# Performance work log

Hardware: AMD Instinct MI355X
Metric: run time of the kernel (lower is better)

Reference implementation:

```python
import jax, jax.numpy as jnp
import numpy as np
import math

WP, WF = 10, 10      # past/future window
EPS = 1e-8           # torch cosine_similarity eps
CLIP = 1.0 - 1e-6    # keep arccos (and its grad) finite
MAXN = 110           # hard-coded alpha width in the module


def setup_inputs() -> dict:
    key = jax.random.key(0)
    k1, k2, k3, k4, k5, k6 = jax.random.split(key, 6)
    B, L, G, N, D = 32, 110, 512, 40, 300
    node_features = jax.random.normal(k1, (B, L, G), jnp.float32)
    knowledge = jax.random.normal(k2, (B, L, N, D), jnp.float32)
    anew = jax.random.uniform(k3, (B, L, N), jnp.float32)
    var_sem = 2.0 / (G + G)
    var_con = 2.0 / (D + D)
    weight_sem = jax.random.normal(k4, (G, G), jnp.float32) * var_sem
    weight_con = jax.random.normal(k5, (D, D), jnp.float32) * var_con
    text_len = jax.random.randint(k6, (B,), 55, L + 1, jnp.int32)
    return dict(node_features=node_features, knowledge=knowledge, anew=anew,
                weight_sem=weight_sem, weight_con=weight_con, text_len=text_len)


def reference(node_features, knowledge, anew, weight_sem, weight_con, text_len):
    B, L, G = node_features.shape
    N = knowledge.shape[2]
    dt = node_features.dtype

    # window + validity mask, replaces per-(i,j) python slicing: [B, j, k]
    j = jnp.arange(L)[:, None]
    k = jnp.arange(L)[None, :]
    cur = text_len[:, None, None]
    mask = (k >= j - WP) & (k <= j + WF)
    mask = mask[None] & (k[None, :, :] <= cur - 1) & (j[None, :, :] < cur)
    fmask = mask.astype(dt)

    # ---- semantic branch: score = 1 - acos(cos_sim(f_j, W_sem f_k))/pi, windowed softmax
    att_sem = jnp.einsum('st,blt->bls', weight_sem, node_features)      # [B,L,G]
    num = jnp.einsum('bjg,bkg->bjk', node_features, att_sem)
    nf = jnp.maximum(jnp.linalg.norm(node_features, axis=-1), EPS)      # [B,L]
    na = jnp.maximum(jnp.linalg.norm(att_sem, axis=-1), EPS)            # [B,L]
    cos = num / (nf[:, :, None] * na[:, None, :])
    score = 1.0 - jnp.arccos(jnp.clip(cos, -CLIP, CLIP)) / math.pi
    neg = jnp.finfo(dt).min
    s = jnp.where(mask, score, neg)
    s = s - jnp.max(s, axis=-1, keepdims=True)
    e = jnp.exp(s) * fmask
    alphas_sem = e / jnp.maximum(jnp.sum(e, axis=-1, keepdims=True), EPS)  # [B,L,L]

    # ---- affinity transform of anew: v -> (||[v, v/2] - [0.5, 0]|| - 0.06467)/0.607468
    anew_aff = (jnp.sqrt((anew - 0.5) ** 2 + (0.5 * anew) ** 2) - 0.06467) / 0.607468

    # ---- contextual branch: windowed sum_n |cos_sim(aff_feat_{k,n}, knowledge_{j,n})|
    att_con = jnp.einsum('blns,st->blnt', knowledge, weight_con)        # [B,L,N,D]
    aff_feat = att_con * anew_aff[..., None]                            # [B,L,N,D]
    num_c = jnp.einsum('bknd,bjnd->bjkn', aff_feat, knowledge)          # [B,j,k,N]
    n_f = jnp.maximum(jnp.linalg.norm(aff_feat, axis=-1), EPS)          # [B,k,N]
    n_k = jnp.maximum(jnp.linalg.norm(knowledge, axis=-1), EPS)         # [B,j,N]
    cos_c = num_c / (n_f[:, None, :, :] * n_k[:, :, None, :])
    alphas_con = 10.0 * jnp.sum(jnp.abs(cos_c), axis=-1) * fmask        # [B,j,k]

    out = 0.5 * alphas_sem + 0.5 * alphas_con                           # [B,L,L]
    if L < MAXN:  # module hard-codes width 110
        out = jnp.pad(out, ((0, 0), (0, 0), (0, MAXN - L)))
    return out
```

## Files before the change

### kernel.cpp

```cpp
#include <hip/hip_runtime.h>
#include <hip/hip_bf16.h>
#include <math.h>

constexpr int Bb   = 32;
constexpr int Ls   = 110;
constexpr int Gs   = 512;
constexpr int Ns   = 40;
constexpr int Ds   = 300;
constexpr int WPc  = 10;
constexpr int WFc  = 10;
constexpr int MAXNc = 110;
constexpr float EPSf  = 1e-8f;
constexpr float CLIPf = 1.0f - 1e-6f;
constexpr int BL = Bb * Ls;
constexpr int Mrows = BL * Ns;

typedef __attribute__((ext_vector_type(8))) short short8_t;
typedef __attribute__((ext_vector_type(4))) short short4_t;
typedef __attribute__((ext_vector_type(4))) float floatx4;

__device__ __forceinline__ unsigned short bf16r(float f) {
  unsigned u = __float_as_uint(f);
  u += 0x7fffu + ((u >> 16) & 1u);
  return (unsigned short)(u >> 16);
}

__global__ __launch_bounds__(256) void transpose_wsem(const float* __restrict__ w,
                                                      float* __restrict__ wt) {
  __shared__ float tile[32][33];
  const int bx = blockIdx.x * 32;
  const int by = blockIdx.y * 32;
  const int tx = threadIdx.x;
  const int ty = threadIdx.y;
#pragma unroll
  for (int r = ty; r < 32; r += 8)
    tile[r][tx] = w[(by + r) * Gs + (bx + tx)];
  __syncthreads();
#pragma unroll
  for (int r = ty; r < 32; r += 8)
    wt[(bx + r) * Gs + (by + tx)] = tile[tx][r];
}

__global__ __launch_bounds__(256) void wct_prep(const float* __restrict__ wc,
                                                short* __restrict__ wct) {
  __shared__ float tile[32][33];
  const int t0 = blockIdx.x * 32;
  const int s0 = blockIdx.y * 32;
  const int tx = threadIdx.x, ty = threadIdx.y;
#pragma unroll
  for (int r = ty; r < 32; r += 8) {
    const int s = s0 + r, t = t0 + tx;
    tile[r][tx] = (s < Ds && t < Ds) ? wc[s * Ds + t] : 0.f;
  }
  __syncthreads();
#pragma unroll
  for (int r = ty; r < 32; r += 8) {
    const int t = t0 + r, s = s0 + tx;
    wct[t * 320 + s] = (short)bf16r(tile[tx][r]);
  }
}

__global__ __launch_bounds__(512) void sem_gemm(const float* __restrict__ nf,
                                                const float* __restrict__ wt,
                                                float* __restrict__ att_sem,
                                                float* __restrict__ na_arr) {
  const int bl0 = blockIdx.x * 8;
  const int s = threadIdx.x;
  const float* __restrict__ x0 = nf + (size_t)bl0 * Gs;
  float acc[8];
#pragma unroll
  for (int r = 0; r < 8; ++r) acc[r] = 0.f;
#pragma unroll 4
  for (int t = 0; t < Gs; ++t) {
    const float wv = wt[t * Gs + s];
#pragma unroll
    for (int r = 0; r < 8; ++r) acc[r] = fmaf(wv, x0[r * Gs + t], acc[r]);
  }
#pragma unroll
  for (int r = 0; r < 8; ++r) att_sem[(size_t)(bl0 + r) * Gs + s] = acc[r];

  __shared__ float partial[8][8];
  const int wave = s >> 6, lane = s & 63;
#pragma unroll
  for (int r = 0; r < 8; ++r) {
    float v = acc[r] * acc[r];
#pragma unroll
    for (int off = 32; off > 0; off >>= 1) v += __shfl_xor(v, off);
    if (lane == 0) partial[r][wave] = v;
  }
  __syncthreads();
  if (s < 8) {
    float sum = 0.f;
#pragma unroll
    for (int w2 = 0; w2 < 8; ++w2) sum += partial[s][w2];
    na_arr[bl0 + s] = fmaxf(sqrtf(sum), EPSf);
  }
}

__global__ __launch_bounds__(256) void sem_attn(const float* __restrict__ nf,
                                                const float* __restrict__ att_sem,
                                                const float* __restrict__ na_arr,
                                                const int* __restrict__ tlen,
                                                float* __restrict__ out) {
  const int blk = blockIdx.x;
  const int b = blk / Ls, j = blk % Ls;
  const int len = tlen[b];
  float* __restrict__ orow = out + (size_t)(b * Ls + j) * MAXNc;
  if (j >= len) {
    for (int k = threadIdx.x; k < MAXNc; k += 256) orow[k] = 0.f;
    return;
  }
  const int k0 = max(j - WPc, 0);
  const int k1 = min(j + WFc, len - 1);
  const int nk = k1 - k0 + 1;

  __shared__ float xs[Gs];
  __shared__ float sc[21];
  __shared__ float red[4];

  const float* __restrict__ x = nf + (size_t)(b * Ls + j) * Gs;
  float ss = 0.f;
  for (int t = threadIdx.x; t < Gs; t += 256) {
    const float v = x[t];
    xs[t] = v;
    ss += v * v;
  }
  const int wave = threadIdx.x >> 6, lane = threadIdx.x & 63;
#pragma unroll
  for (int off = 32; off > 0; off >>= 1) ss += __shfl_xor(ss, off);
  if (lane == 0) red[wave] = ss;
  __syncthreads();
  const float nfn = fmaxf(sqrtf(red[0] + red[1] + red[2] + red[3]), EPSf);

  for (int i = wave; i < nk; i += 4) {
    const int k = k0 + i;
    const float* __restrict__ as = att_sem + (size_t)(b * Ls + k) * Gs;
    float d = 0.f;
#pragma unroll
    for (int t = lane; t < Gs; t += 64) d = fmaf(xs[t], as[t], d);
#pragma unroll
    for (int off = 32; off > 0; off >>= 1) d += __shfl_xor(d, off);
    if (lane == 0) {
      float cs = d / (nfn * na_arr[b * Ls + k]);
      cs = fminf(fmaxf(cs, -CLIPf), CLIPf);
      sc[i] = 1.0f - acosf(cs) * (float)(1.0 / M_PI);
    }
  }
  __syncthreads();
  if (threadIdx.x == 0) {
    float m = -1e30f;
    for (int i = 0; i < nk; ++i) m = fmaxf(m, sc[i]);
    red[0] = m;
  }
  __syncthreads();
  const float m = red[0];
  if ((int)threadIdx.x < nk) sc[threadIdx.x] = expf(sc[threadIdx.x] - m);
  __syncthreads();
  if (threadIdx.x == 0) {
    float s = 0.f;
    for (int i = 0; i < nk; ++i) s += sc[i];
    red[1] = 1.0f / fmaxf(s, EPSf);
  }
  __syncthreads();
  const float inv = red[1];
  for (int k = threadIdx.x; k < MAXNc; k += 256) {
    float v = 0.f;
    if (k >= k0 && k <= k1) v = 0.5f * sc[k - k0] * inv;
    orow[k] = v;
  }
}

__global__ __launch_bounds__(256) void con_gemm_mfma(const float* __restrict__ kn,
                                                     const short* __restrict__ wct,
                                                     const float* __restrict__ anew,
                                                     const int* __restrict__ tlen,
                                                     unsigned short* __restrict__ ybar) {
  const int row0 = blockIdx.x * 64;
  {
    const int bl0 = row0 / Ns, bl1 = (row0 + 63) / Ns;
    bool alive = false;
    for (int bl = bl0; bl <= bl1; ++bl)
      if ((bl % Ls) < tlen[bl / Ls]) alive = true;
    if (!alive) return;
  }

  __shared__ short A_lds[64 * 40];
  __shared__ float rowss[64][4];
  __shared__ float scl[64];

  const int tid = threadIdx.x;
  const int wave = tid >> 6, lane = tid & 63;
  const int quad = lane >> 4, l16 = lane & 15;

  floatx4 acc[4][5];
#pragma unroll
  for (int mt = 0; mt < 4; ++mt)
#pragma unroll
    for (int i = 0; i < 5; ++i) acc[mt][i] = (floatx4){0.f, 0.f, 0.f, 0.f};

  const int r_st = tid >> 3;
  const int pos = tid & 7;

  for (int c = 0; c < 10; ++c) {
    const int k0 = c * 32 + pos * 4;
#pragma unroll
    for (int half = 0; half < 2; ++half) {
      const int r = r_st + half * 32;
      float4 v = make_float4(0.f, 0.f, 0.f, 0.f);
      if (k0 < Ds)
        v = *reinterpret_cast<const float4*>(kn + (size_t)(row0 + r) * Ds + k0);
      short4_t p;
      p.x = (short)bf16r(v.x);
      p.y = (short)bf16r(v.y);
      p.z = (short)bf16r(v.z);
      p.w = (short)bf16r(v.w);
      *reinterpret_cast<short4_t*>(&A_lds[r * 40 + pos * 4]) = p;
    }
    __syncthreads();

    short8_t bfrag[5];
#pragma unroll
    for (int i = 0; i < 5; ++i) {
      const int t = wave * 80 + i * 16 + l16;
      bfrag[i] = *reinterpret_cast<const short8_t*>(wct + t * 320 + c * 32 + quad * 8);
    }
#pragma unroll
    for (int mt = 0; mt < 4; ++mt) {
      const short8_t afrag =
          *reinterpret_cast<const short8_t*>(&A_lds[(mt * 16 + l16) * 40 + quad * 8]);
#pragma unroll
      for (int i = 0; i < 5; ++i)
        acc[mt][i] = __builtin_amdgcn_mfma_f32_16x16x32_bf16(afrag, bfrag[i], acc[mt][i], 0, 0, 0);
    }
    __syncthreads();
  }

#pragma unroll
  for (int mt = 0; mt < 4; ++mt) {
#pragma unroll
    for (int r = 0; r < 4; ++r) {
      float p = 0.f;
#pragma unroll
      for (int i = 0; i < 5; ++i) {
        const float y = acc[mt][i][r];
        p = fmaf(y, y, p);
      }
      p += __shfl_xor(p, 1);
      p += __shfl_xor(p, 2);
      p += __shfl_xor(p, 4);
      p += __shfl_xor(p, 8);
      if (l16 == 0) rowss[mt * 16 + quad * 4 + r][wave] = p;
    }
  }
  __syncthreads();
  if (tid < 64) {
    const float ss = rowss[tid][0] + rowss[tid][1] + rowss[tid][2] + rowss[tid][3];
    const float a = anew[row0 + tid];
    const float aff = (sqrtf((a - 0.5f) * (a - 0.5f) + 0.25f * a * a) - 0.06467f) *
                      (1.0f / 0.607468f);
    scl[tid] = aff / fmaxf(aff * sqrtf(ss), EPSf);
  }
  __syncthreads();

#pragma unroll
  for (int mt = 0; mt < 4; ++mt) {
#pragma unroll
    for (int i = 0; i < 5; ++i) {
      const int col = wave * 80 + i * 16 + l16;
      if (col < Ds) {
#pragma unroll
        for (int r = 0; r < 4; ++r) {
          const int row = mt * 16 + quad * 4 + r;
          ybar[(size_t)(row0 + row) * Ds + col] = bf16r(acc[mt][i][r] * scl[row]);
        }
      }
    }
  }
}

__global__ __launch_bounds__(512) void con_attn_mfma(const float* __restrict__ kn,
                                                     const unsigned short* __restrict__ ybar,
                                                     const int* __restrict__ tlen,
                                                     float* __restrict__ out) {
  const int b = blockIdx.x / 7;
  const int jt = blockIdx.x % 7;
  const int j0 = jt * 16;
  const int len = tlen[b];
  if (j0 >= len) return;
  const int kbase = min(max(j0 - WPc, 0), Ls - 48);

  const int tid = threadIdx.x;
  const int wave = tid >> 6, lane = tid & 63;
  const int quad = lane >> 4, l16 = lane & 15;

  __shared__ float red[8][768];

  const int jj = min(j0 + l16, Ls - 1);
  const size_t blj = (size_t)(b * Ls + jj);

  float outacc[3][4];
#pragma unroll
  for (int t = 0; t < 3; ++t)
#pragma unroll
    for (int r = 0; r < 4; ++r) outacc[t][r] = 0.f;

  const unsigned short* yrow[3];
#pragma unroll
  for (int t = 0; t < 3; ++t) {
    const int k = kbase + t * 16 + l16;
    yrow[t] = ybar + ((size_t)(b * Ls + k) * Ns) * Ds;
  }

  for (int ni = 0; ni < 5; ++ni) {
    const int n = wave + ni * 8;
    const float* __restrict__ arow = kn + (blj * Ns + n) * Ds;

    floatx4 S[3];
#pragma unroll
    for (int t = 0; t < 3; ++t) S[t] = (floatx4){0.f, 0.f, 0.f, 0.f};
    float ssq = 0.f;

#pragma unroll
    for (int c = 0; c < 10; ++c) {
      const int d0 = c * 32 + quad * 8;
      float av[8];
      if (c < 9) {
        const float4 v0 = *reinterpret_cast<const float4*>(arow + d0);
        const float4 v1 = *reinterpret_cast<const float4*>(arow + d0 + 4);
        av[0] = v0.x; av[1] = v0.y; av[2] = v0.z; av[3] = v0.w;
        av[4] = v1.x; av[5] = v1.y; av[6] = v1.z; av[7] = v1.w;
      } else {
        if (quad == 0) {
          const float4 v0 = *reinterpret_cast<const float4*>(arow + d0);
          const float4 v1 = *reinterpret_cast<const float4*>(arow + d0 + 4);
          av[0] = v0.x; av[1] = v0.y; av[2] = v0.z; av[3] = v0.w;
          av[4] = v1.x; av[5] = v1.y; av[6] = v1.z; av[7] = v1.w;
        } else if (quad == 1) {
          const float4 v0 = *reinterpret_cast<const float4*>(arow + d0);
          av[0] = v0.x; av[1] = v0.y; av[2] = v0.z; av[3] = v0.w;
          av[4] = av[5] = av[6] = av[7] = 0.f;
        } else {
#pragma unroll
          for (int e = 0; e < 8; ++e) av[e] = 0.f;
        }
      }
      short8_t afrag;
#pragma unroll
      for (int e = 0; e < 8; ++e) {
        ssq = fmaf(av[e], av[e], ssq);
        afrag[e] = (short)bf16r(av[e]);
      }
#pragma unroll
      for (int t = 0; t < 3; ++t) {
        const unsigned short* yr = yrow[t] + (size_t)n * Ds;
        short8_t bfrag;
        if (c < 9) {
          const short4_t u0 = *reinterpret_cast<const short4_t*>(yr + d0);
          const short4_t u1 = *reinterpret_cast<const short4_t*>(yr + d0 + 4);
          bfrag[0] = u0.x; bfrag[1] = u0.y; bfrag[2] = u0.z; bfrag[3] = u0.w;
          bfrag[4] = u1.x; bfrag[5] = u1.y; bfrag[6] = u1.z; bfrag[7] = u1.w;
        } else {
          if (quad == 0) {
            const short4_t u0 = *reinterpret_cast<const short4_t*>(yr + d0);
            const short4_t u1 = *reinterpret_cast<const short4_t*>(yr + d0 + 4);
            bfrag[0] = u0.x; bfrag[1] = u0.y; bfrag[2] = u0.z; bfrag[3] = u0.w;
            bfrag[4] = u1.x; bfrag[5] = u1.y; bfrag[6] = u1.z; bfrag[7] = u1.w;
          } else if (quad == 1) {
            const short4_t u0 = *reinterpret_cast<const short4_t*>(yr + d0);
            bfrag[0] = u0.x; bfrag[1] = u0.y; bfrag[2] = u0.z; bfrag[3] = u0.w;
            bfrag[4] = bfrag[5] = bfrag[6] = bfrag[7] = 0;
          } else {
#pragma unroll
            for (int e = 0; e < 8; ++e) bfrag[e] = 0;
          }
        }
        S[t] = __builtin_amdgcn_mfma_f32_16x16x32_bf16(afrag, bfrag, S[t], 0, 0, 0);
      }
    }

    ssq += __shfl_xor(ssq, 16);
    ssq += __shfl_xor(ssq, 32);
    const float kinv = 1.0f / fmaxf(sqrtf(ssq), EPSf);

#pragma unroll
    for (int r = 0; r < 4; ++r) {
      const float kv = __shfl(kinv, quad * 4 + r);
#pragma unroll
      for (int t = 0; t < 3; ++t)
        outacc[t][r] = fmaf(kv, fabsf(S[t][r]), outacc[t][r]);
    }
  }

#pragma unroll
  for (int t = 0; t < 3; ++t)
#pragma unroll
    for (int r = 0; r < 4; ++r)
      red[wave][(quad * 4 + r) * 48 + t * 16 + l16] = outacc[t][r];
  __syncthreads();

  for (int idx = tid; idx < 768; idx += 512) {
    float s = 0.f;
#pragma unroll
    for (int w = 0; w < 8; ++w) s += red[w][idx];
    const int j = j0 + idx / 48;
    const int k = kbase + idx % 48;
    if (j < len && k < len && k >= j - WPc && k <= j + WFc)
      out[(size_t)(b * Ls + j) * MAXNc + k] += 5.0f * s;
  }
}

extern "C" void kernel_launch(void* const* d_in, const int* in_sizes, int n_in,
                              void* d_out, int out_size, void* d_ws, size_t ws_size,
                              hipStream_t stream) {
  const float* nf   = (const float*)d_in[0];
  const float* kn   = (const float*)d_in[1];
  const float* anew = (const float*)d_in[2];
  const float* wsem = (const float*)d_in[3];
  const float* wcon = (const float*)d_in[4];
  const int*   tlen = (const int*)d_in[5];
  float* out = (float*)d_out;

  float* att_sem = (float*)d_ws;
  float* na_arr  = att_sem + (size_t)BL * Gs;
  float* wt      = na_arr + BL;
  short* wct     = (short*)(wt + (size_t)Gs * Gs);
  unsigned short* ybar = (unsigned short*)(wct + 320 * 320);

  transpose_wsem<<<dim3(16, 16), dim3(32, 8), 0, stream>>>(wsem, wt);
  wct_prep<<<dim3(10, 10), dim3(32, 8), 0, stream>>>(wcon, wct);
  sem_gemm<<<BL / 8, 512, 0, stream>>>(nf, wt, att_sem, na_arr);
  sem_attn<<<BL, 256, 0, stream>>>(nf, att_sem, na_arr, tlen, out);
  con_gemm_mfma<<<Mrows / 64, 256, 0, stream>>>(kn, wct, anew, tlen, ybar);
  con_attn_mfma<<<Bb * 7, 512, 0, stream>>>(kn, ybar, tlen, out);
}
```

Before: 508.2 us.

## Load con GEMM A fragments directly from global, drop LDS staging and barriers

The contextual GEMM kernel no longer stages the knowledge rows in shared memory. Each wave now loads its A fragments straight from global memory as float4 pairs and converts them to packed bf16 in registers. The K loop is split into nine full chunks plus a masked tail chunk, which removes both __syncthreads per iteration. In exchange, all four waves now redundantly read the same A rows from global/L2, and the per-lane loads are less coalesced.

```diff
diff --git a/kernel.cpp b/kernel.cpp
--- a/kernel.cpp
+++ b/kernel.cpp
@@ -25,6 +25,22 @@
   return (unsigned short)(u >> 16);
 }
 
+__device__ __forceinline__ unsigned pkbf(float lo, float hi) {
+  unsigned a = __float_as_uint(lo), b = __float_as_uint(hi);
+  a += 0x7fffu + ((a >> 16) & 1u);
+  b += 0x7fffu + ((b >> 16) & 1u);
+  return (a >> 16) | (b & 0xffff0000u);
+}
+
+__device__ __forceinline__ short8_t cvt8(const float4 v0, const float4 v1) {
+  union { short8_t s; unsigned u[4]; } p;
+  p.u[0] = pkbf(v0.x, v0.y);
+  p.u[1] = pkbf(v0.z, v0.w);
+  p.u[2] = pkbf(v1.x, v1.y);
+  p.u[3] = pkbf(v1.z, v1.w);
+  return p.s;
+}
+
 __global__ __launch_bounds__(256) void transpose_wsem(const float* __restrict__ w,
                                                       float* __restrict__ wt) {
   __shared__ float tile[32][33];
@@ -184,7 +200,6 @@
     if (!alive) return;
   }
 
-  __shared__ short A_lds[64 * 40];
   __shared__ float rowss[64][4];
   __shared__ float scl[64];
 
@@ -198,41 +213,54 @@
 #pragma unroll
     for (int i = 0; i < 5; ++i) acc[mt][i] = (floatx4){0.f, 0.f, 0.f, 0.f};
 
-  const int r_st = tid >> 3;
-  const int pos = tid & 7;
-
-  for (int c = 0; c < 10; ++c) {
-    const int k0 = c * 32 + pos * 4;
-#pragma unroll
-    for (int half = 0; half < 2; ++half) {
-      const int r = r_st + half * 32;
-      float4 v = make_float4(0.f, 0.f, 0.f, 0.f);
-      if (k0 < Ds)
-        v = *reinterpret_cast<const float4*>(kn + (size_t)(row0 + r) * Ds + k0);
-      short4_t p;
-      p.x = (short)bf16r(v.x);
-      p.y = (short)bf16r(v.y);
-      p.z = (short)bf16r(v.z);
-      p.w = (short)bf16r(v.w);
-      *reinterpret_cast<short4_t*>(&A_lds[r * 40 + pos * 4]) = p;
-    }
-    __syncthreads();
-
+  const float* arow[4];
+#pragma unroll
+  for (int mt = 0; mt < 4; ++mt)
+    arow[mt] = kn + (size_t)(row0 + mt * 16 + l16) * Ds;
+
+  const short* brow[5];
+#pragma unroll
+  for (int i = 0; i < 5; ++i)
+    brow[i] = wct + (wave * 80 + i * 16 + l16) * 320 + quad * 8;
+
+  for (int c = 0; c < 9; ++c) {
+    const int d0 = c * 32 + quad * 8;
     short8_t bfrag[5];
 #pragma unroll
-    for (int i = 0; i < 5; ++i) {
-      const int t = wave * 80 + i * 16 + l16;
-      bfrag[i] = *reinterpret_cast<const short8_t*>(wct + t * 320 + c * 32 + quad * 8);
-    }
+    for (int i = 0; i < 5; ++i)
+      bfrag[i] = *reinterpret_cast<const short8_t*>(brow[i] + c * 32);
 #pragma unroll
     for (int mt = 0; mt < 4; ++mt) {
-      const short8_t afrag =
-          *reinterpret_cast<const short8_t*>(&A_lds[(mt * 16 + l16) * 40 + quad * 8]);
+      const float4 v0 = *reinterpret_cast<const float4*>(arow[mt] + d0);
+      const float4 v1 = *reinterpret_cast<const float4*>(arow[mt] + d0 + 4);
+      const short8_t afrag = cvt8(v0, v1);
 #pragma unroll
       for (int i = 0; i < 5; ++i)
         acc[mt][i] = __builtin_amdgcn_mfma_f32_16x16x32_bf16(afrag, bfrag[i], acc[mt][i], 0, 0, 0);
     }
-    __syncthreads();
+  }
+
+  {
+    const int d0 = 288 + quad * 8;
+    short8_t bfrag[5];
+#pragma unroll
+    for (int i = 0; i < 5; ++i)
+      bfrag[i] = *reinterpret_cast<const short8_t*>(brow[i] + 288);
+#pragma unroll
+    for (int mt = 0; mt < 4; ++mt) {
+      float4 v0 = make_float4(0.f, 0.f, 0.f, 0.f);
+      float4 v1 = make_float4(0.f, 0.f, 0.f, 0.f);
+      if (quad == 0) {
+        v0 = *reinterpret_cast<const float4*>(arow[mt] + d0);
+        v1 = *reinterpret_cast<const float4*>(arow[mt] + d0 + 4);
+      } else if (quad == 1) {
+        v0 = *reinterpret_cast<const float4*>(arow[mt] + d0);
+      }
+      const short8_t afrag = cvt8(v0, v1);
+#pragma unroll
+      for (int i = 0; i < 5; ++i)
+        acc[mt][i] = __builtin_amdgcn_mfma_f32_16x16x32_bf16(afrag, bfrag[i], acc[mt][i], 0, 0, 0);
+    }
   }
 
 #pragma unroll
```

Measured after the change: 541.7 us. 6.6% more time.
